# Kernel optimization log

Measured on AMD Instinct MI355X. Metric: run time of the kernel, lower is better.

The kernel has to match this reference:

```python
import jax, jax.numpy as jnp
import numpy as np


def _next_pow2(n: int) -> int:
    # matches torch: 2 ** ceil(log2(n))
    return 1 << (int(n) - 1).bit_length()


def setup_inputs() -> dict:
    key = jax.random.key(0)
    k1, k2 = jax.random.split(key)
    B, T, L = 256, 32768, 32768
    x = jax.random.normal(k1, (B, T), dtype=jnp.float32)
    filt = jax.random.normal(k2, (1, L), dtype=jnp.float32)
    return {"x": x, "filt": filt}


def reference(x, filt):
    """EpochedFutureFill.forward: exact causal convolution of x with filt.

    The per-token epoched algorithm (tau-step direct sum + FutureFill FFT
    cache refresh every K steps, cache initialized to zero) computes exactly
    y[b, t] = sum_{s=0}^{min(t, L-1)} filt[0, s] * x[b, t-s].
    We compute it with one FFT-based linear convolution, mirroring the
    float32 FFT math of future_fill().
    """
    B, T = x.shape
    L = filt.shape[-1]
    n_fft = _next_pow2(T + L - 1)
    xf = jnp.fft.rfft(x.astype(jnp.float32), n=n_fft)          # (B, n_fft//2+1)
    wf = jnp.fft.rfft(filt.astype(jnp.float32), n=n_fft)       # (1, n_fft//2+1)
    y = jnp.fft.irfft(xf * wf, n=n_fft)[:, :T]                 # causal lags 0..T-1
    return y.astype(x.dtype)
```

## Files before the change

kernel.cpp:

```cpp
#include <hip/hip_runtime.h>
#include <cstdint>

typedef __attribute__((ext_vector_type(8))) short short8;
typedef __attribute__((ext_vector_type(4))) float floatx4;

#define TWO_PI 6.283185307179586f

__device__ __forceinline__ unsigned short f2bf(float f) {
  union { float f; uint32_t u; } c; c.f = f;
  uint32_t u = c.u;
  u += 0x7FFFu + ((u >> 16) & 1u);
  return (unsigned short)(u >> 16);
}
__device__ __forceinline__ uint32_t packbf(float re, float im) {
  return (uint32_t)f2bf(re) | ((uint32_t)f2bf(im) << 16);
}


__global__ __launch_bounds__(256) void prep_all(
    const float* __restrict__ x, const float* __restrict__ filt,
    unsigned short* __restrict__ A1, unsigned short* __restrict__ A2,
    unsigned short* __restrict__ A3, unsigned short* __restrict__ A4,
    uint32_t* __restrict__ Zp, float2* __restrict__ Gw) {
  const int bid = blockIdx.x;
  const int tid = threadIdx.x;
  const float w256 = TWO_PI / 256.0f;
  if (bid < 3072) {
    int idx = bid * 256 + tid;
    if (idx < 131072) {
      int col = idx & 255, row = idx >> 8;
      int k1 = row >> 1, d = row & 1, r = col >> 1, e = col & 1;
      float th = (float)((k1 * r) & 255) * w256;
      float sn, cs; __sincosf(th, &sn, &cs);
      A1[idx] = f2bf(d == 0 ? (e == 0 ? cs : sn) : (e == 0 ? -sn : cs));
    } else if (idx < 393216) {
      int j = idx - 131072;
      int col = j & 511, row = j >> 9;
      int k2 = row >> 1, d = row & 1, cc = col >> 1, e = col & 1;
      float th = (float)((k2 * cc) & 255) * w256;
      float sn, cs; __sincosf(th, &sn, &cs);
      A2[j] = f2bf(d == 0 ? (e == 0 ? cs : sn) : (e == 0 ? -sn : cs));
    } else if (idx < 655360) {
      int j = idx - 393216;
      int col = j & 511, row = j >> 9;
      int cc = row >> 1, d = row & 1, k2 = col >> 1, e = col & 1;
      float th = (float)((k2 * cc) & 255) * w256;
      float sn, cs; __sincosf(th, &sn, &cs);
      A3[j] = f2bf(d == 0 ? (e == 0 ? cs : -sn) : (e == 0 ? sn : cs));
    } else {
      int j = idx - 655360;
      int col = j & 511, row = j >> 9;
      int r = row >> 1, d = row & 1, k1 = col >> 1, e = col & 1;
      float th = (float)((k1 * r) & 255) * w256;
      float sn, cs; __sincosf(th, &sn, &cs);
      A4[j] = f2bf(d == 0 ? (e == 0 ? cs : -sn) : (e == 0 ? sn : cs));
    }
  } else if (bid < 4096) {
    int b2 = bid - 3072;
    int s = b2 >> 3, rq = b2 & 7;
    const float* x0 = x + (size_t)(2 * s) * 32768;
    const float* x1 = x0 + 32768;
    uint32_t v[16];
    #pragma unroll
    for (int rr = 0; rr < 16; ++rr) {
      int t = tid + 256 * (rq * 16 + rr);
      v[rr] = (uint32_t)f2bf(x0[t]) | ((uint32_t)f2bf(x1[t]) << 16);
    }
    uint32_t* dst = Zp + (size_t)(s * 256 + tid) * 128 + rq * 16;
    #pragma unroll
    for (int j = 0; j < 16; j += 4)
      *(uint4*)(dst + j) = make_uint4(v[j], v[j + 1], v[j + 2], v[j + 3]);
  } else {
    int k1 = bid - 4096, c = tid;
    float ar = 0.f, ai = 0.f;
    for (int r = 0; r < 128; ++r) {
      float v = filt[c + 256 * r];
      float th = (float)((k1 * r) & 255) * w256;
      float sn, cs; __sincosf(th, &sn, &cs);
      ar += v * cs; ai -= v * sn;
    }
    float th = (float)((k1 * c) & 65535) * (TWO_PI / 65536.0f);
    float sn, cs; __sincosf(th, &sn, &cs);
    Gw[(k1 << 8) + c] = make_float2(ar * cs + ai * sn, ai * cs - ar * sn);
  }
}

__global__ __launch_bounds__(256) void prep_wb(const float2* __restrict__ Gw,
                                               float2* __restrict__ WtT) {
  int k1 = blockIdx.x, k2 = threadIdx.x;
  float ar = 0.f, ai = 0.f;
  for (int c = 0; c < 256; ++c) {
    float2 g = Gw[(k1 << 8) + c];
    float th = (float)((k2 * c) & 255) * (TWO_PI / 256.0f);
    float sn, cs; __sincosf(th, &sn, &cs);
    ar += g.x * cs + g.y * sn;
    ai += g.y * cs - g.x * sn;
  }
  WtT[(k2 << 8) + k1] = make_float2(ar, ai);
}

template <int MODE, int KITERS>
__global__ __launch_bounds__(256, 2) void dft_stage(
    const unsigned short* __restrict__ Af,
    const unsigned short* __restrict__ Bd,
    uint32_t* __restrict__ outp,
    float* __restrict__ yout,
    const float2* __restrict__ WtT) {
  __shared__ unsigned short Sm[32768];
  constexpr int KP = KITERS * 64;

  const int mt = blockIdx.x >> 8;
  const int nt = blockIdx.x & 255;
  const int m0 = mt * 128, n0 = nt * 128;

  const int tid = threadIdx.x;
  const int w = tid >> 6, lane = tid & 63;
  const int qlo = lane & 15, qhi = lane >> 4;
  const int wr = w >> 1, wc = w & 1;
  const int r8 = lane >> 3, pl = lane & 7, sj = pl ^ r8, q3 = qlo & 7;

  floatx4 acc[4][4];
  #pragma unroll
  for (int i = 0; i < 4; ++i)
    #pragma unroll
    for (int j = 0; j < 4; ++j) acc[i][j] = (floatx4){0.f, 0.f, 0.f, 0.f};

  auto issue = [&](int it, int buf) {
    const int k0 = it * 64;
    unsigned short* Asb = Sm + buf * 8192;
    unsigned short* Bsb = Sm + 16384 + buf * 8192;
    #pragma unroll
    for (int q = 0; q < 4; ++q) {
      const int R = w * 32 + q * 8 + r8;
      const unsigned short* gA = Af + (size_t)(m0 + R) * KP + k0 + sj * 8;
      const unsigned short* gB = Bd + (size_t)(n0 + R) * KP + k0 + sj * 8;
      __builtin_amdgcn_global_load_lds(
          (const __attribute__((address_space(1))) uint32_t*)gA,
          (__attribute__((address_space(3))) uint32_t*)&Asb[(w * 32 + q * 8) * 64], 16, 0, 0);
      __builtin_amdgcn_global_load_lds(
          (const __attribute__((address_space(1))) uint32_t*)gB,
          (__attribute__((address_space(3))) uint32_t*)&Bsb[(w * 32 + q * 8) * 64], 16, 0, 0);
    }
  };

  issue(0, 0);
  for (int it = 0; it < KITERS; ++it) {
    __syncthreads();
    if (it + 1 < KITERS) issue(it + 1, (it + 1) & 1);
    const unsigned short* Ab = Sm + (it & 1) * 8192;
    const unsigned short* Bb = Sm + 16384 + (it & 1) * 8192;
    #pragma unroll
    for (int ks = 0; ks < 2; ++ks) {
      short8 a[4], bb[4];
      #pragma unroll
      for (int im = 0; im < 4; ++im) {
        const int R = wr * 64 + im * 16 + qlo;
        a[im] = *(const short8*)&Ab[R * 64 + (((ks * 4 + qhi) ^ q3) << 3)];
      }
      #pragma unroll
      for (int in = 0; in < 4; ++in) {
        const int R = wc * 64 + in * 16 + qlo;
        bb[in] = *(const short8*)&Bb[R * 64 + (((ks * 4 + qhi) ^ q3) << 3)];
      }
      #pragma unroll
      for (int im = 0; im < 4; ++im)
        #pragma unroll
        for (int in = 0; in < 4; ++in)
          acc[im][in] = __builtin_amdgcn_mfma_f32_16x16x32_bf16(a[im], bb[in], acc[im][in], 0, 0, 0);
    }
  }

  const int s_idx = n0 >> 8;
  const int cl0 = n0 & 255;

  if (MODE == 2) {
    __syncthreads();
    uint32_t* Tr = (uint32_t*)Sm;
    #pragma unroll
    for (int im = 0; im < 4; ++im) {
      const int mloc = wr * 32 + im * 8 + qhi * 2;
      #pragma unroll
      for (int in = 0; in < 4; ++in) {
        const int nloc = wc * 64 + in * 16 + qlo;
        #pragma unroll
        for (int pp = 0; pp < 2; ++pp) {
          const int mC = (m0 >> 1) + mloc + pp;
          float re = acc[im][in][2 * pp], iv = acc[im][in][2 * pp + 1];
          float2 wv = WtT[(mC << 8) + cl0 + nloc];
          float r2 = re * wv.x - iv * wv.y, i2 = re * wv.y + iv * wv.x;
          Tr[nloc * 68 + mloc + pp] = packbf(r2, i2);
        }
      }
    }
    __syncthreads();
    const int ln = tid >> 1, half = tid & 1;
    uint32_t* dst = outp + (size_t)((s_idx << 8) + cl0 + ln) * 256 + (m0 >> 1) + half * 32;
    const uint32_t* srcp = Tr + ln * 68 + half * 32;
    #pragma unroll
    for (int j = 0; j < 32; j += 4)
      *(uint4*)(dst + j) = *(const uint4*)(srcp + j);
    return;
  }

  #pragma unroll
  for (int im = 0; im < 4; ++im) {
    const int mloc = wr * 32 + im * 8 + qhi * 2;
    #pragma unroll
    for (int in = 0; in < 4; ++in) {
      const int nloc = wc * 64 + in * 16 + qlo;
      const int cloc = cl0 + nloc;
      #pragma unroll
      for (int pp = 0; pp < 2; ++pp) {
        const int mC = (m0 >> 1) + mloc + pp;
        float re = acc[im][in][2 * pp], iv = acc[im][in][2 * pp + 1];
        if (MODE == 1) {
          float th = (float)((mC * cloc) & 65535) * (TWO_PI / 65536.0f);
          float sn, cs; __sincosf(th, &sn, &cs);
          float r2 = re * cs + iv * sn, i2 = iv * cs - re * sn;
          outp[(size_t)((s_idx << 8) + mC) * 256 + cloc] = packbf(r2, i2);
        } else if (MODE == 3) {
          float th = (float)((mC * cloc) & 65535) * (TWO_PI / 65536.0f);
          float sn, cs; __sincosf(th, &sn, &cs);
          float r2 = re * cs - iv * sn, i2 = iv * cs + re * sn;
          outp[(size_t)((s_idx << 8) + mC) * 256 + cloc] = packbf(r2, i2);
        } else {
          const float sc = 1.0f / 65536.0f;
          float* y0 = yout + ((size_t)s_idx << 16) + (mC << 8) + cloc;
          y0[0] = re * sc;
          y0[32768] = iv * sc;
        }
      }
    }
  }
}

extern "C" void kernel_launch(void* const* d_in, const int* in_sizes, int n_in,
                              void* d_out, int out_size, void* d_ws, size_t ws_size,
                              hipStream_t stream) {
  const float* x = (const float*)d_in[0];
  const float* filt = (const float*)d_in[1];
  float* Y = (float*)d_out;

  char* ws = (char*)d_ws;
  unsigned short* A1 = (unsigned short*)(ws + 0);
  unsigned short* A2 = (unsigned short*)(ws + 0x40000);
  unsigned short* A3 = (unsigned short*)(ws + 0xC0000);
  unsigned short* A4 = (unsigned short*)(ws + 0x140000);
  float2* Gw  = (float2*)(ws + 0x180000);
  float2* WtT = (float2*)(ws + 0x200000);
  unsigned short* Zp = (unsigned short*)(ws + (3u << 20));
  unsigned short* G2 = (unsigned short*)(ws + 19922944u);
  unsigned short* P  = (unsigned short*)(ws + 53477376u);
  unsigned short* H2 = (unsigned short*)(ws + (3u << 20));

  hipLaunchKernelGGL(prep_all, dim3(4352), dim3(256), 0, stream,
                     x, filt, A1, A2, A3, A4, (uint32_t*)Zp, Gw);
  hipLaunchKernelGGL(prep_wb, dim3(256), dim3(256), 0, stream, Gw, WtT);

  hipLaunchKernelGGL((dft_stage<1, 4>), dim3(1024), dim3(256), 0, stream,
                     A1, Zp, (uint32_t*)G2, (float*)nullptr, (const float2*)nullptr);
  hipLaunchKernelGGL((dft_stage<2, 8>), dim3(1024), dim3(256), 0, stream,
                     A2, G2, (uint32_t*)P, (float*)nullptr, WtT);
  hipLaunchKernelGGL((dft_stage<3, 8>), dim3(1024), dim3(256), 0, stream,
                     A3, P, (uint32_t*)H2, (float*)nullptr, (const float2*)nullptr);
  hipLaunchKernelGGL((dft_stage<4, 8>), dim3(512), dim3(256), 0, stream,
                     A4, H2, (uint32_t*)nullptr, Y, (const float2*)nullptr);
}
```

Before: 194.0 us.

## Prepack DFT twiddle matrices in MFMA fragment order and widen N tile to 256

The DFT twiddle matrices are now precomputed in the exact per-lane MFMA operand layout, so each wave loads its A fragments straight from global memory (L2-resident) instead of staging them through LDS. Each block now covers a 64x256 output tile (every wave does 8x4 MFMA tiles over a 64-column slice), which halves grid sizes and doubles B tile reuse in LDS. This removes A-tile LDS traffic and the associated sync pressure. In exchange it raises accumulator register use and relies on cache hits for A loads that are not overlapped through LDS double buffering.

```diff
diff --git a/kernel.cpp b/kernel.cpp
--- a/kernel.cpp
+++ b/kernel.cpp
@@ -16,6 +16,18 @@
   return (uint32_t)f2bf(re) | ((uint32_t)f2bf(im) << 16);
 }
 
+
+__device__ __forceinline__ float amat_val(int which, int m, int k) {
+  const float w256 = TWO_PI / 256.0f;
+  int a = m >> 1, d = m & 1, b = k >> 1, e = k & 1;
+  float th = (float)((a * b) & 255) * w256;
+  float sn, cs; __sincosf(th, &sn, &cs);
+  if (which <= 2) {
+    return d == 0 ? (e == 0 ? cs : sn) : (e == 0 ? -sn : cs);
+  } else {
+    return d == 0 ? (e == 0 ? cs : -sn) : (e == 0 ? sn : cs);
+  }
+}
 
 __global__ __launch_bounds__(256) void prep_all(
     const float* __restrict__ x, const float* __restrict__ filt,
@@ -24,37 +36,24 @@
     uint32_t* __restrict__ Zp, float2* __restrict__ Gw) {
   const int bid = blockIdx.x;
   const int tid = threadIdx.x;
-  const float w256 = TWO_PI / 256.0f;
   if (bid < 3072) {
     int idx = bid * 256 + tid;
-    if (idx < 131072) {
-      int col = idx & 255, row = idx >> 8;
-      int k1 = row >> 1, d = row & 1, r = col >> 1, e = col & 1;
-      float th = (float)((k1 * r) & 255) * w256;
-      float sn, cs; __sincosf(th, &sn, &cs);
-      A1[idx] = f2bf(d == 0 ? (e == 0 ? cs : sn) : (e == 0 ? -sn : cs));
-    } else if (idx < 393216) {
-      int j = idx - 131072;
-      int col = j & 511, row = j >> 9;
-      int k2 = row >> 1, d = row & 1, cc = col >> 1, e = col & 1;
-      float th = (float)((k2 * cc) & 255) * w256;
-      float sn, cs; __sincosf(th, &sn, &cs);
-      A2[j] = f2bf(d == 0 ? (e == 0 ? cs : sn) : (e == 0 ? -sn : cs));
-    } else if (idx < 655360) {
-      int j = idx - 393216;
-      int col = j & 511, row = j >> 9;
-      int cc = row >> 1, d = row & 1, k2 = col >> 1, e = col & 1;
-      float th = (float)((k2 * cc) & 255) * w256;
-      float sn, cs; __sincosf(th, &sn, &cs);
-      A3[j] = f2bf(d == 0 ? (e == 0 ? cs : -sn) : (e == 0 ? sn : cs));
-    } else {
-      int j = idx - 655360;
-      int col = j & 511, row = j >> 9;
-      int r = row >> 1, d = row & 1, k1 = col >> 1, e = col & 1;
-      float th = (float)((k1 * r) & 255) * w256;
-      float sn, cs; __sincosf(th, &sn, &cs);
-      A4[j] = f2bf(d == 0 ? (e == 0 ? cs : -sn) : (e == 0 ? sn : cs));
-    }
+    int which, local, KIT;
+    unsigned short* dst;
+    if (idx < 131072)      { which = 1; local = idx;          KIT = 4; dst = A1; }
+    else if (idx < 393216) { which = 2; local = idx - 131072; KIT = 8; dst = A2; }
+    else if (idx < 655360) { which = 3; local = idx - 393216; KIT = 8; dst = A3; }
+    else                   { which = 4; local = idx - 655360; KIT = 8; dst = A4; }
+    int j    = local & 7;
+    int lane = (local >> 3) & 63;
+    int qlo = lane & 15, qhi = lane >> 4;
+    int im   = (local >> 9) & 7;
+    int ks   = (local >> 12) & 1;
+    int rest = local >> 13;
+    int it = rest % KIT, mt = rest / KIT;
+    int m = mt * 128 + im * 16 + qlo;
+    int k = it * 64 + ks * 32 + qhi * 8 + j;
+    dst[local] = f2bf(amat_val(which, m, k));
   } else if (bid < 4096) {
     int b2 = bid - 3072;
     int s = b2 >> 3, rq = b2 & 7;
@@ -75,7 +74,7 @@
     float ar = 0.f, ai = 0.f;
     for (int r = 0; r < 128; ++r) {
       float v = filt[c + 256 * r];
-      float th = (float)((k1 * r) & 255) * w256;
+      float th = (float)((k1 * r) & 255) * (TWO_PI / 256.0f);
       float sn, cs; __sincosf(th, &sn, &cs);
       ar += v * cs; ai -= v * sn;
     }
@@ -106,126 +105,110 @@
     uint32_t* __restrict__ outp,
     float* __restrict__ yout,
     const float2* __restrict__ WtT) {
-  __shared__ unsigned short Sm[32768];
+  __shared__ unsigned short Sm[34816];
   constexpr int KP = KITERS * 64;
 
-  const int mt = blockIdx.x >> 8;
-  const int nt = blockIdx.x & 255;
-  const int m0 = mt * 128, n0 = nt * 128;
+  const int nt = blockIdx.x & 127;
+  const int mt = blockIdx.x >> 7;
+  const int n0 = nt * 256;
 
   const int tid = threadIdx.x;
   const int w = tid >> 6, lane = tid & 63;
   const int qlo = lane & 15, qhi = lane >> 4;
-  const int wr = w >> 1, wc = w & 1;
   const int r8 = lane >> 3, pl = lane & 7, sj = pl ^ r8, q3 = qlo & 7;
 
-  floatx4 acc[4][4];
+  floatx4 acc[8][4];
   #pragma unroll
-  for (int i = 0; i < 4; ++i)
+  for (int i = 0; i < 8; ++i)
     #pragma unroll
     for (int j = 0; j < 4; ++j) acc[i][j] = (floatx4){0.f, 0.f, 0.f, 0.f};
 
-  auto issue = [&](int it, int buf) {
+  auto issueB = [&](int it, int buf) {
     const int k0 = it * 64;
-    unsigned short* Asb = Sm + buf * 8192;
-    unsigned short* Bsb = Sm + 16384 + buf * 8192;
-    #pragma unroll
-    for (int q = 0; q < 4; ++q) {
-      const int R = w * 32 + q * 8 + r8;
-      const unsigned short* gA = Af + (size_t)(m0 + R) * KP + k0 + sj * 8;
+    unsigned short* Bsb = Sm + buf * 16384;
+    #pragma unroll
+    for (int q = 0; q < 8; ++q) {
+      const int R = w * 64 + q * 8 + r8;
       const unsigned short* gB = Bd + (size_t)(n0 + R) * KP + k0 + sj * 8;
       __builtin_amdgcn_global_load_lds(
-          (const __attribute__((address_space(1))) uint32_t*)gA,
-          (__attribute__((address_space(3))) uint32_t*)&Asb[(w * 32 + q * 8) * 64], 16, 0, 0);
-      __builtin_amdgcn_global_load_lds(
           (const __attribute__((address_space(1))) uint32_t*)gB,
-          (__attribute__((address_space(3))) uint32_t*)&Bsb[(w * 32 + q * 8) * 64], 16, 0, 0);
+          (__attribute__((address_space(3))) uint32_t*)&Bsb[(w * 64 + q * 8) * 64], 16, 0, 0);
     }
   };
 
-  issue(0, 0);
+  issueB(0, 0);
   for (int it = 0; it < KITERS; ++it) {
     __syncthreads();
-    if (it + 1 < KITERS) issue(it + 1, (it + 1) & 1);
-    const unsigned short* Ab = Sm + (it & 1) * 8192;
-    const unsigned short* Bb = Sm + 16384 + (it & 1) * 8192;
+    if (it + 1 < KITERS) issueB(it + 1, (it + 1) & 1);
+    const unsigned short* Bb = Sm + (it & 1) * 16384;
+    const unsigned short* Ab = Af + (size_t)((mt * KITERS + it) * 2) * 8 * 512;
     #pragma unroll
     for (int ks = 0; ks < 2; ++ks) {
-      short8 a[4], bb[4];
-      #pragma unroll
-      for (int im = 0; im < 4; ++im) {
-        const int R = wr * 64 + im * 16 + qlo;
-        a[im] = *(const short8*)&Ab[R * 64 + (((ks * 4 + qhi) ^ q3) << 3)];
-      }
-      #pragma unroll
-      for (int in = 0; in < 4; ++in) {
-        const int R = wc * 64 + in * 16 + qlo;
-        bb[in] = *(const short8*)&Bb[R * 64 + (((ks * 4 + qhi) ^ q3) << 3)];
-      }
-      #pragma unroll
-      for (int im = 0; im < 4; ++im)
+      short8 a[8], bb[4];
+      #pragma unroll
+      for (int im = 0; im < 8; ++im)
+        a[im] = *(const short8*)(Ab + ((ks * 8 + im) << 9) + (lane << 3));
+      #pragma unroll
+      for (int in = 0; in < 4; ++in)
+        bb[in] = *(const short8*)&Bb[(w * 64 + in * 16 + qlo) * 64 + (((ks * 4 + qhi) ^ q3) << 3)];
+      #pragma unroll
+      for (int im = 0; im < 8; ++im)
         #pragma unroll
         for (int in = 0; in < 4; ++in)
           acc[im][in] = __builtin_amdgcn_mfma_f32_16x16x32_bf16(a[im], bb[in], acc[im][in], 0, 0, 0);
     }
   }
 
-  const int s_idx = n0 >> 8;
-  const int cl0 = n0 & 255;
-
   if (MODE == 2) {
     __syncthreads();
     uint32_t* Tr = (uint32_t*)Sm;
     #pragma unroll
-    for (int im = 0; im < 4; ++im) {
-      const int mloc = wr * 32 + im * 8 + qhi * 2;
+    for (int im = 0; im < 8; ++im) {
       #pragma unroll
       for (int in = 0; in < 4; ++in) {
-        const int nloc = wc * 64 + in * 16 + qlo;
+        const int nloc = w * 64 + in * 16 + qlo;
         #pragma unroll
         for (int pp = 0; pp < 2; ++pp) {
-          const int mC = (m0 >> 1) + mloc + pp;
+          const int mloc = im * 8 + qhi * 2 + pp;
+          const int mC = mt * 64 + mloc;
           float re = acc[im][in][2 * pp], iv = acc[im][in][2 * pp + 1];
-          float2 wv = WtT[(mC << 8) + cl0 + nloc];
+          float2 wv = WtT[(mC << 8) + nloc];
           float r2 = re * wv.x - iv * wv.y, i2 = re * wv.y + iv * wv.x;
-          Tr[nloc * 68 + mloc + pp] = packbf(r2, i2);
+          Tr[nloc * 68 + mloc] = packbf(r2, i2);
         }
       }
     }
     __syncthreads();
-    const int ln = tid >> 1, half = tid & 1;
-    uint32_t* dst = outp + (size_t)((s_idx << 8) + cl0 + ln) * 256 + (m0 >> 1) + half * 32;
-    const uint32_t* srcp = Tr + ln * 68 + half * 32;
-    #pragma unroll
-    for (int j = 0; j < 32; j += 4)
+    uint32_t* dst = outp + (size_t)((nt << 8) + tid) * 256 + mt * 64;
+    const uint32_t* srcp = Tr + tid * 68;
+    #pragma unroll
+    for (int j = 0; j < 64; j += 4)
       *(uint4*)(dst + j) = *(const uint4*)(srcp + j);
     return;
   }
 
   #pragma unroll
-  for (int im = 0; im < 4; ++im) {
-    const int mloc = wr * 32 + im * 8 + qhi * 2;
+  for (int im = 0; im < 8; ++im) {
     #pragma unroll
     for (int in = 0; in < 4; ++in) {
-      const int nloc = wc * 64 + in * 16 + qlo;
-      const int cloc = cl0 + nloc;
+      const int nloc = w * 64 + in * 16 + qlo;
       #pragma unroll
       for (int pp = 0; pp < 2; ++pp) {
-        const int mC = (m0 >> 1) + mloc + pp;
+        const int mC = mt * 64 + im * 8 + qhi * 2 + pp;
         float re = acc[im][in][2 * pp], iv = acc[im][in][2 * pp + 1];
         if (MODE == 1) {
-          float th = (float)((mC * cloc) & 65535) * (TWO_PI / 65536.0f);
+          float th = (float)((mC * nloc) & 65535) * (TWO_PI / 65536.0f);
           float sn, cs; __sincosf(th, &sn, &cs);
           float r2 = re * cs + iv * sn, i2 = iv * cs - re * sn;
-          outp[(size_t)((s_idx << 8) + mC) * 256 + cloc] = packbf(r2, i2);
+          outp[(size_t)((nt << 8) + mC) * 256 + nloc] = packbf(r2, i2);
         } else if (MODE == 3) {
-          float th = (float)((mC * cloc) & 65535) * (TWO_PI / 65536.0f);
+          float th = (float)((mC * nloc) & 65535) * (TWO_PI / 65536.0f);
           float sn, cs; __sincosf(th, &sn, &cs);
           float r2 = re * cs - iv * sn, i2 = iv * cs + re * sn;
-          outp[(size_t)((s_idx << 8) + mC) * 256 + cloc] = packbf(r2, i2);
+          outp[(size_t)((nt << 8) + mC) * 256 + nloc] = packbf(r2, i2);
         } else {
           const float sc = 1.0f / 65536.0f;
-          float* y0 = yout + ((size_t)s_idx << 16) + (mC << 8) + cloc;
+          float* y0 = yout + ((size_t)nt << 16) + (mC << 8) + nloc;
           y0[0] = re * sc;
           y0[32768] = iv * sc;
         }
@@ -257,12 +240,12 @@
                      x, filt, A1, A2, A3, A4, (uint32_t*)Zp, Gw);
   hipLaunchKernelGGL(prep_wb, dim3(256), dim3(256), 0, stream, Gw, WtT);
 
-  hipLaunchKernelGGL((dft_stage<1, 4>), dim3(1024), dim3(256), 0, stream,
+  hipLaunchKernelGGL((dft_stage<1, 4>), dim3(512), dim3(256), 0, stream,
                      A1, Zp, (uint32_t*)G2, (float*)nullptr, (const float2*)nullptr);
-  hipLaunchKernelGGL((dft_stage<2, 8>), dim3(1024), dim3(256), 0, stream,
+  hipLaunchKernelGGL((dft_stage<2, 8>), dim3(512), dim3(256), 0, stream,
                      A2, G2, (uint32_t*)P, (float*)nullptr, WtT);
-  hipLaunchKernelGGL((dft_stage<3, 8>), dim3(1024), dim3(256), 0, stream,
+  hipLaunchKernelGGL((dft_stage<3, 8>), dim3(512), dim3(256), 0, stream,
                      A3, P, (uint32_t*)H2, (float*)nullptr, (const float2*)nullptr);
-  hipLaunchKernelGGL((dft_stage<4, 8>), dim3(512), dim3(256), 0, stream,
+  hipLaunchKernelGGL((dft_stage<4, 8>), dim3(256), dim3(256), 0, stream,
                      A4, H2, (uint32_t*)nullptr, Y, (const float2*)nullptr);
 }
```

Result: slower. 217.6 us (+12.1%).
